# Performance work log

Measured on AMD Instinct MI355X. Metric: run time of the kernel, lower is better.

## Reference

```python
import jax, jax.numpy as jnp
import numpy as np
from jax import lax

B, S = 4, 2048
HIDDEN = 1024
OUT = 1024
NUM_TABLE = 64
CODE_LEN = 10
TABLE_SIZE = 2 ** CODE_LEN  # 1024
TOTAL_DIM = NUM_TABLE * CODE_LEN  # 640


def setup_inputs() -> dict:
    key = jax.random.key(0)
    k1, k2, k3, k4, k5 = jax.random.split(key, 5)
    hidden_states = jax.random.normal(k1, (B, S, HIDDEN), dtype=jnp.float32)
    # nn.Linear(hidden_size, total_dim): weight [total_dim, hidden] in torch; store as [hidden, total_dim]
    W_proj = jax.random.normal(k2, (HIDDEN, TOTAL_DIM), dtype=jnp.float32) * (1.0 / np.sqrt(HIDDEN))
    b_proj = jax.random.normal(k3, (TOTAL_DIM,), dtype=jnp.float32) * 0.01
    tables = 0.02 * jax.random.normal(k4, (NUM_TABLE * TABLE_SIZE, OUT), dtype=jnp.float32)
    bias = 0.001 * jax.random.normal(k5, (OUT,), dtype=jnp.float32)
    return {"hidden_states": hidden_states, "W_proj": W_proj, "b_proj": b_proj,
            "tables": tables, "bias": bias}


def reference(hidden_states, W_proj, b_proj, tables, bias):
    other_shape = hidden_states.shape[:-1]
    x = hidden_states.reshape(-1, HIDDEN)  # [N, H], N = B*S
    # Hashing: dense projection then per-table code/score
    z = x @ W_proj + b_proj                       # [N, total_dim]
    z = z.reshape(-1, NUM_TABLE, CODE_LEN)        # [N, T, L]
    t = jnp.tanh(jnp.abs(z))
    score = jnp.prod((1.0 + t) * 0.5, axis=-1)    # [N, T] prob of selected bucket
    pow2 = (2 ** jnp.arange(CODE_LEN, dtype=jnp.int32))
    code = jnp.sum((z > 0).astype(jnp.int32) * pow2, axis=-1)  # [N, T] in [0, TABLE_SIZE)

    # Gather + weighted sum over tables, streamed with scan to avoid [N, T, OUT]
    tabs = tables.reshape(NUM_TABLE, TABLE_SIZE, OUT)
    code_t = code.T    # [T, N]
    score_t = score.T  # [T, N]

    def body(acc, inp):
        tab, idx, w = inp  # tab [TABLE_SIZE, OUT], idx [N], w [N]
        return acc + tab[idx] * w[:, None], None

    acc0 = jnp.zeros((x.shape[0], OUT), dtype=hidden_states.dtype)
    out, _ = lax.scan(body, acc0, (tabs, code_t, score_t))
    out = out + bias
    return out.reshape(*other_shape, OUT)
```

## Files before the change

### kernel.cpp

```cpp
#include <hip/hip_runtime.h>
#include <cstddef>
#include <cstdint>

#define HIDDEN    1024
#define OUTD      1024
#define NUM_TABLE 64
#define CODE_LEN  10
#define TABLE_SZ  1024
#define TOTAL_DIM 640

#define TAU   1e-3f
#define FCAP  65536u

typedef float  fx4    __attribute__((ext_vector_type(4)));
typedef ushort ux4    __attribute__((ext_vector_type(4)));
typedef ushort ux8    __attribute__((ext_vector_type(8)));
typedef short  bf16x8 __attribute__((ext_vector_type(8)));
typedef float  f32x4  __attribute__((ext_vector_type(4)));

struct bfp { ushort hi, lo; };
static __device__ __forceinline__ bfp split2(float v) {
    uint32_t u  = __float_as_uint(v);
    float    fh = __uint_as_float(u & 0xFFFF0000u);
    uint32_t ul = __float_as_uint(v - fh);
    bfp r; r.hi = (ushort)(u >> 16); r.lo = (ushort)(ul >> 16);
    return r;
}
static __device__ __forceinline__ ushort f2bf(float f) {
    uint32_t u = __float_as_uint(f);
    return (ushort)((u + 0x7FFFu + ((u >> 16) & 1u)) >> 16);
}

__global__ __launch_bounds__(256)
void split_wt(const float* __restrict__ W, ushort* __restrict__ wht, ushort* __restrict__ wlt)
{
    __shared__ float t[32][33];
    const int d0 = blockIdx.x * 32, k0 = blockIdx.y * 32;
    const int lx = threadIdx.x & 31, ly = threadIdx.x >> 5;
    #pragma unroll
    for (int i = 0; i < 32; i += 8)
        t[ly + i][lx] = W[(size_t)(k0 + ly + i) * TOTAL_DIM + d0 + lx];
    __syncthreads();
    #pragma unroll
    for (int i = 0; i < 32; i += 8) {
        bfp s = split2(t[lx][ly + i]);
        size_t o = (size_t)(d0 + ly + i) * HIDDEN + k0 + lx;
        wht[o] = s.hi; wlt[o] = s.lo;
    }
}

#define GBM 128
#define GBN 128
#define GBK 32
#define LDK 40

__global__ __launch_bounds__(256)
void gemm_mfma(const float* __restrict__ x, const ushort* __restrict__ wht,
               const ushort* __restrict__ wlt, const float* __restrict__ bproj,
               float* __restrict__ z)
{
    __shared__ ushort Ah[GBM][LDK];
    __shared__ ushort Al[GBM][LDK];
    __shared__ ushort Bh[GBN][LDK];
    __shared__ ushort Bl[GBN][LDK];

    const int tid  = threadIdx.x;
    const int lane = tid & 63, wid = tid >> 6;
    const int wr = wid >> 1, wc = wid & 1;
    const int brow = blockIdx.x * GBM;
    const int bcol = blockIdx.y * GBN;
    const int fr = lane & 15, fq = lane >> 4;

    f32x4 acc[4][4] = {};

    for (int k0 = 0; k0 < HIDDEN; k0 += GBK) {
        #pragma unroll
        for (int i = 0; i < 4; ++i) {
            int c = tid + i * 256;
            int r = c >> 3, kc = (c & 7) * 4;
            fx4 v = *(const fx4*)&x[(size_t)(brow + r) * HIDDEN + k0 + kc];
            bfp s0 = split2(v.x), s1 = split2(v.y), s2 = split2(v.z), s3 = split2(v.w);
            ux4 h, l;
            h.x = s0.hi; l.x = s0.lo;
            h.y = s1.hi; l.y = s1.lo;
            h.z = s2.hi; l.z = s2.lo;
            h.w = s3.hi; l.w = s3.lo;
            *(ux4*)&Ah[r][kc] = h;
            *(ux4*)&Al[r][kc] = l;
        }
        #pragma unroll
        for (int i = 0; i < 2; ++i) {
            int c = tid + i * 256;
            int nr = c >> 2, kc = (c & 3) * 8;
            size_t o = (size_t)(bcol + nr) * HIDDEN + k0 + kc;
            *(ux8*)&Bh[nr][kc] = *(const ux8*)&wht[o];
            *(ux8*)&Bl[nr][kc] = *(const ux8*)&wlt[o];
        }
        __syncthreads();

        bf16x8 ah[4], al[4], bh[4], bl[4];
        #pragma unroll
        for (int m = 0; m < 4; ++m) {
            ah[m] = *(const bf16x8*)&Ah[wr * 64 + m * 16 + fr][fq * 8];
            al[m] = *(const bf16x8*)&Al[wr * 64 + m * 16 + fr][fq * 8];
        }
        #pragma unroll
        for (int n = 0; n < 4; ++n) {
            bh[n] = *(const bf16x8*)&Bh[wc * 64 + n * 16 + fr][fq * 8];
            bl[n] = *(const bf16x8*)&Bl[wc * 64 + n * 16 + fr][fq * 8];
        }
        #pragma unroll
        for (int m = 0; m < 4; ++m)
            #pragma unroll
            for (int n = 0; n < 4; ++n) {
                acc[m][n] = __builtin_amdgcn_mfma_f32_16x16x32_bf16(ah[m], bh[n], acc[m][n], 0, 0, 0);
                acc[m][n] = __builtin_amdgcn_mfma_f32_16x16x32_bf16(ah[m], bl[n], acc[m][n], 0, 0, 0);
                acc[m][n] = __builtin_amdgcn_mfma_f32_16x16x32_bf16(al[m], bh[n], acc[m][n], 0, 0, 0);
            }
        __syncthreads();
    }

    #pragma unroll
    for (int n = 0; n < 4; ++n) {
        int col = bcol + wc * 64 + n * 16 + fr;
        float bb = bproj[col];
        #pragma unroll
        for (int m = 0; m < 4; ++m) {
            int rbase = brow + wr * 64 + m * 16 + fq * 4;
            #pragma unroll
            for (int j = 0; j < 4; ++j)
                z[(size_t)(rbase + j) * TOTAL_DIM + col] = acc[m][n][j] + bb;
        }
    }
}

__global__ __launch_bounds__(256)
void code_score2(const float* __restrict__ z, int* __restrict__ code,
                 float* __restrict__ score, uint32_t* __restrict__ flags,
                 uint32_t* __restrict__ cnt, int NT)
{
    int idx = blockIdx.x * 256 + threadIdx.x;
    if (idx >= NT) return;
    int n = idx >> 6;
    int t = idx & 63;
    const float* zp = z + (size_t)n * TOTAL_DIM + t * CODE_LEN;
    float s = 1.0f;
    int   c = 0;
    #pragma unroll
    for (int i = 0; i < CODE_LEN; ++i) {
        float v = zp[i];
        if (fabsf(v) < TAU) {
            uint32_t slot = atomicAdd(cnt, 1u);
            if (slot < FCAP) flags[slot] = (uint32_t)(n * TOTAL_DIM + t * CODE_LEN + i);
        }
        s *= 0.5f * (1.0f + tanhf(fabsf(v)));
        c |= (v > 0.0f) ? (1 << i) : 0;
    }
    code[idx]  = c;
    score[idx] = s;
}

__global__ __launch_bounds__(256)
void fixz(const float* __restrict__ x, const float* __restrict__ W,
          const float* __restrict__ bproj, const float* __restrict__ z,
          int* __restrict__ code, const uint32_t* __restrict__ flags,
          const uint32_t* __restrict__ cnt)
{
    const int lane = threadIdx.x & 63;
    const int gw   = (blockIdx.x * 256 + threadIdx.x) >> 6;
    const int nw   = (gridDim.x * 256) >> 6;
    uint32_t count = *cnt;
    if (count > FCAP) count = FCAP;

    for (uint32_t f = gw; f < count; f += nw) {
        uint32_t e = flags[f];
        int n = e / TOTAL_DIM, d = e % TOTAL_DIM;
        const float* xr = x + (size_t)n * HIDDEN;
        float p = 0.0f;
        #pragma unroll
        for (int j = 0; j < 16; ++j) {
            int k = lane + j * 64;
            p = fmaf(xr[k], W[(size_t)k * TOTAL_DIM + d], p);
        }
        #pragma unroll
        for (int off = 32; off; off >>= 1) p += __shfl_xor(p, off);
        float v = p + bproj[d];
        if (lane == 0) {
            float vold = z[e];
            if ((v > 0.0f) != (vold > 0.0f)) {
                int t = d / CODE_LEN, i = d % CODE_LEN;
                atomicXor(&code[n * NUM_TABLE + t], 1 << i);
            }
        }
    }
}

__global__ __launch_bounds__(256)
void convert_tables(const float* __restrict__ t, ushort* __restrict__ o, int n4)
{
    const fx4* tp = (const fx4*)t;
    int stride = gridDim.x * 256;
    for (int i = blockIdx.x * 256 + threadIdx.x; i < n4; i += stride) {
        fx4 v = __builtin_nontemporal_load(&tp[i]);
        ux4 u;
        u.x = f2bf(v.x); u.y = f2bf(v.y); u.z = f2bf(v.z); u.w = f2bf(v.w);
        *(ux4*)&o[(size_t)i * 4] = u;
    }
}

__global__ __launch_bounds__(256)
void gather_sum_bf16(const ushort* __restrict__ btab, const float* __restrict__ bias,
                     const int* __restrict__ code, const float* __restrict__ score,
                     float* __restrict__ out)
{
    __shared__ int   sc[NUM_TABLE];
    __shared__ float sw[NUM_TABLE];

    const int n   = blockIdx.x;
    const int tid = threadIdx.x;

    if (tid < NUM_TABLE) {
        sc[tid] = code[n * NUM_TABLE + tid];
        sw[tid] = score[n * NUM_TABLE + tid];
    }
    __syncthreads();

    float4 acc = *(const float4*)&bias[tid * 4];

    #pragma unroll 4
    for (int t = 0; t < NUM_TABLE; ++t) {
        const ux4 v = *(const ux4*)&btab[((size_t)(t * TABLE_SZ + sc[t])) * OUTD + tid * 4];
        float w = sw[t];
        acc.x += w * __uint_as_float((uint32_t)v.x << 16);
        acc.y += w * __uint_as_float((uint32_t)v.y << 16);
        acc.z += w * __uint_as_float((uint32_t)v.z << 16);
        acc.w += w * __uint_as_float((uint32_t)v.w << 16);
    }

    *(float4*)&out[(size_t)n * OUTD + tid * 4] = acc;
}

#define BM 64
#define BN 64
#define BK 32
__global__ __launch_bounds__(256)
void gemm_proj(const float* __restrict__ x, const float* __restrict__ W,
               const float* __restrict__ bproj, float* __restrict__ z)
{
    __shared__ float As[BK][BM + 4];
    __shared__ float Bs[BK][BN];
    const int tid  = threadIdx.x;
    const int brow = blockIdx.x * BM;
    const int bcol = blockIdx.y * BN;
    const int tr   = tid >> 4;
    const int tc   = tid & 15;
    float acc[4][4] = {};
    for (int k0 = 0; k0 < HIDDEN; k0 += BK) {
        #pragma unroll
        for (int i = 0; i < 2; ++i) {
            int lin = tid + i * 256;
            int r = lin >> 3, c8 = lin & 7;
            float4 a = *(const float4*)&x[(size_t)(brow + r) * HIDDEN + k0 + c8 * 4];
            As[c8 * 4 + 0][r] = a.x; As[c8 * 4 + 1][r] = a.y;
            As[c8 * 4 + 2][r] = a.z; As[c8 * 4 + 3][r] = a.w;
        }
        #pragma unroll
        for (int i = 0; i < 2; ++i) {
            int lin = tid + i * 256;
            int kk = lin >> 4, m4 = lin & 15;
            *(float4*)&Bs[kk][m4 * 4] =
                *(const float4*)&W[(size_t)(k0 + kk) * TOTAL_DIM + bcol + m4 * 4];
        }
        __syncthreads();
        #pragma unroll
        for (int kk = 0; kk < BK; ++kk) {
            float4 a = *(const float4*)&As[kk][tr * 4];
            float4 b = *(const float4*)&Bs[kk][tc * 4];
            acc[0][0] += a.x * b.x; acc[0][1] += a.x * b.y; acc[0][2] += a.x * b.z; acc[0][3] += a.x * b.w;
            acc[1][0] += a.y * b.x; acc[1][1] += a.y * b.y; acc[1][2] += a.y * b.z; acc[1][3] += a.y * b.w;
            acc[2][0] += a.z * b.x; acc[2][1] += a.z * b.y; acc[2][2] += a.z * b.z; acc[2][3] += a.z * b.w;
            acc[3][0] += a.w * b.x; acc[3][1] += a.w * b.y; acc[3][2] += a.w * b.z; acc[3][3] += a.w * b.w;
        }
        __syncthreads();
    }
    float4 bb = *(const float4*)&bproj[bcol + tc * 4];
    #pragma unroll
    for (int i = 0; i < 4; ++i) {
        int r = brow + tr * 4 + i;
        float4 o = {acc[i][0] + bb.x, acc[i][1] + bb.y, acc[i][2] + bb.z, acc[i][3] + bb.w};
        *(float4*)&z[(size_t)r * TOTAL_DIM + bcol + tc * 4] = o;
    }
}

__global__ __launch_bounds__(256)
void code_score(const float* __restrict__ z, int* __restrict__ code,
                float* __restrict__ score, int NT)
{
    int idx = blockIdx.x * 256 + threadIdx.x;
    if (idx >= NT) return;
    int n = idx >> 6, t = idx & 63;
    const float* zp = z + (size_t)n * TOTAL_DIM + t * CODE_LEN;
    float s = 1.0f; int c = 0;
    #pragma unroll
    for (int i = 0; i < CODE_LEN; ++i) {
        float v = zp[i];
        s *= 0.5f * (1.0f + tanhf(fabsf(v)));
        c |= (v > 0.0f) ? (1 << i) : 0;
    }
    code[idx] = c; score[idx] = s;
}

__global__ __launch_bounds__(256)
void gather_sum_f32(const float* __restrict__ tables, const float* __restrict__ bias,
                    const int* __restrict__ code, const float* __restrict__ score,
                    float* __restrict__ out)
{
    __shared__ int   sc[NUM_TABLE];
    __shared__ float sw[NUM_TABLE];
    const int n = blockIdx.x, tid = threadIdx.x;
    if (tid < NUM_TABLE) {
        sc[tid] = code[n * NUM_TABLE + tid];
        sw[tid] = score[n * NUM_TABLE + tid];
    }
    __syncthreads();
    float4 acc = *(const float4*)&bias[tid * 4];
    #pragma unroll 4
    for (int t = 0; t < NUM_TABLE; ++t) {
        const float* row = tables + ((size_t)(t * TABLE_SZ + sc[t])) * OUTD;
        float4 v = *(const float4*)&row[tid * 4];
        float w = sw[t];
        acc.x += v.x * w; acc.y += v.y * w; acc.z += v.z * w; acc.w += v.w * w;
    }
    *(float4*)&out[(size_t)n * OUTD + tid * 4] = acc;
}

extern "C" void kernel_launch(void* const* d_in, const int* in_sizes, int n_in,
                              void* d_out, int out_size, void* d_ws, size_t ws_size,
                              hipStream_t stream) {
    const float* x      = (const float*)d_in[0];
    const float* W      = (const float*)d_in[1];
    const float* bproj  = (const float*)d_in[2];
    const float* tables = (const float*)d_in[3];
    const float* bias   = (const float*)d_in[4];
    float* out = (float*)d_out;

    const int N = in_sizes[0] / HIDDEN;

    char* ws = (char*)d_ws;
    size_t off_z     = 0;
    size_t off_code  = off_z + (size_t)N * TOTAL_DIM * sizeof(float);
    size_t off_score = off_code + (size_t)N * NUM_TABLE * sizeof(int);
    size_t off_btab  = off_score + (size_t)N * NUM_TABLE * sizeof(float);
    size_t tab_elems = (size_t)NUM_TABLE * TABLE_SZ * OUTD;
    size_t need      = off_btab + tab_elems * sizeof(ushort);

    float*  z     = (float*)(ws + off_z);
    int*    code  = (int*)(ws + off_code);
    float*  score = (float*)(ws + off_score);
    ushort* btab  = (ushort*)(ws + off_btab);
    uint32_t* flags = (uint32_t*)(ws + off_btab);
    uint32_t* cnt   = (uint32_t*)(ws + off_btab + (size_t)FCAP * 4);
    ushort*   wht   = (ushort*)(ws + off_btab + (1u << 20));
    ushort*   wlt   = (ushort*)(ws + off_btab + (3u << 20));

    int NT = N * NUM_TABLE;

    if (ws_size >= need) {
        dim3 gw(TOTAL_DIM / 32, HIDDEN / 32);
        split_wt<<<gw, 256, 0, stream>>>(W, wht, wlt);

        dim3 g1(N / GBM, TOTAL_DIM / GBN);
        gemm_mfma<<<g1, 256, 0, stream>>>(x, wht, wlt, bproj, z);

        (void)hipMemsetAsync(cnt, 0, 4, stream);
        code_score2<<<(NT + 255) / 256, 256, 0, stream>>>(z, code, score, flags, cnt, NT);
        fixz<<<512, 256, 0, stream>>>(x, W, bproj, z, code, flags, cnt);

        convert_tables<<<2048, 256, 0, stream>>>(tables, btab, (int)(tab_elems / 4));
        gather_sum_bf16<<<N, 256, 0, stream>>>(btab, bias, code, score, out);
    } else {
        dim3 g1(N / BM, TOTAL_DIM / BN);
        gemm_proj<<<g1, 256, 0, stream>>>(x, W, bproj, z);
        code_score<<<(NT + 255) / 256, 256, 0, stream>>>(z, code, score, NT);
        gather_sum_f32<<<N, 256, 0, stream>>>(tables, bias, code, score, out);
    }
}
```

Baseline: 344.9 us.

## Fuse table conversion into GEMM launch and split gather into column halves

The bf16 table conversion now runs as extra blocks inside the projection GEMM launch, so the memory-bound conversion can overlap the compute-bound GEMM instead of running as a separate kernel. The converted tables are stored as two column halves of 512, and the gather runs as two 128-thread launches, one per half, so each pass touches a smaller working set that may stay in cache. The risks are that conversion blocks compete with the GEMM for CUs, that the gather needs an extra launch and rereads code and score, and that the workspace layout grows.

```diff
diff --git a/kernel.cpp b/kernel.cpp
--- a/kernel.cpp
+++ b/kernel.cpp
@@ -53,22 +53,46 @@
 #define GBN 128
 #define GBK 32
 #define LDK 40
-
-__global__ __launch_bounds__(256)
-void gemm_mfma(const float* __restrict__ x, const ushort* __restrict__ wht,
-               const ushort* __restrict__ wlt, const float* __restrict__ bproj,
-               float* __restrict__ z)
+#define GEMM_MB (8192 / GBM)
+#define GEMM_NB (TOTAL_DIM / GBN)
+#define GEMM_BLKS (GEMM_MB * GEMM_NB)
+#define CONV_BLKS 1024
+
+__global__ __launch_bounds__(256)
+void gemm_convert(const float* __restrict__ x, const ushort* __restrict__ wht,
+                  const ushort* __restrict__ wlt, const float* __restrict__ bproj,
+                  float* __restrict__ z,
+                  const float* __restrict__ tables,
+                  ushort* __restrict__ btabA, ushort* __restrict__ btabB)
 {
     __shared__ ushort Ah[GBM][LDK];
     __shared__ ushort Al[GBM][LDK];
     __shared__ ushort Bh[GBN][LDK];
     __shared__ ushort Bl[GBN][LDK];
 
-    const int tid  = threadIdx.x;
+    const int gb  = blockIdx.x;
+    const int tid = threadIdx.x;
+
+    if (gb >= GEMM_BLKS) {
+        const int n4 = NUM_TABLE * TABLE_SZ * (OUTD / 4);
+        const fx4* tp = (const fx4*)tables;
+        const int stride = CONV_BLKS * 256;
+        for (int i = (gb - GEMM_BLKS) * 256 + tid; i < n4; i += stride) {
+            fx4 v = __builtin_nontemporal_load(&tp[i]);
+            ux4 u;
+            u.x = f2bf(v.x); u.y = f2bf(v.y); u.z = f2bf(v.z); u.w = f2bf(v.w);
+            int row = i >> 8;
+            int cg  = i & 255;
+            if (cg < 128) *(ux4*)&btabA[(size_t)row * 512 + cg * 4]         = u;
+            else          *(ux4*)&btabB[(size_t)row * 512 + (cg - 128) * 4] = u;
+        }
+        return;
+    }
+
     const int lane = tid & 63, wid = tid >> 6;
     const int wr = wid >> 1, wc = wid & 1;
-    const int brow = blockIdx.x * GBM;
-    const int bcol = blockIdx.y * GBN;
+    const int brow = (gb % GEMM_MB) * GBM;
+    const int bcol = (gb / GEMM_MB) * GBN;
     const int fr = lane & 15, fq = lane >> 4;
 
     f32x4 acc[4][4] = {};
@@ -195,23 +219,10 @@
     }
 }
 
-__global__ __launch_bounds__(256)
-void convert_tables(const float* __restrict__ t, ushort* __restrict__ o, int n4)
-{
-    const fx4* tp = (const fx4*)t;
-    int stride = gridDim.x * 256;
-    for (int i = blockIdx.x * 256 + threadIdx.x; i < n4; i += stride) {
-        fx4 v = __builtin_nontemporal_load(&tp[i]);
-        ux4 u;
-        u.x = f2bf(v.x); u.y = f2bf(v.y); u.z = f2bf(v.z); u.w = f2bf(v.w);
-        *(ux4*)&o[(size_t)i * 4] = u;
-    }
-}
-
-__global__ __launch_bounds__(256)
-void gather_sum_bf16(const ushort* __restrict__ btab, const float* __restrict__ bias,
-                     const int* __restrict__ code, const float* __restrict__ score,
-                     float* __restrict__ out)
+__global__ __launch_bounds__(128)
+void gather_half(const ushort* __restrict__ btabH, const float* __restrict__ bias,
+                 const int* __restrict__ code, const float* __restrict__ score,
+                 float* __restrict__ out, int colbase)
 {
     __shared__ int   sc[NUM_TABLE];
     __shared__ float sw[NUM_TABLE];
@@ -225,11 +236,11 @@
     }
     __syncthreads();
 
-    float4 acc = *(const float4*)&bias[tid * 4];
+    float4 acc = *(const float4*)&bias[colbase + tid * 4];
 
     #pragma unroll 4
     for (int t = 0; t < NUM_TABLE; ++t) {
-        const ux4 v = *(const ux4*)&btab[((size_t)(t * TABLE_SZ + sc[t])) * OUTD + tid * 4];
+        const ux4 v = *(const ux4*)&btabH[((size_t)(t * TABLE_SZ + sc[t])) * 512 + tid * 4];
         float w = sw[t];
         acc.x += w * __uint_as_float((uint32_t)v.x << 16);
         acc.y += w * __uint_as_float((uint32_t)v.y << 16);
@@ -237,7 +248,7 @@
         acc.w += w * __uint_as_float((uint32_t)v.w << 16);
     }
 
-    *(float4*)&out[(size_t)n * OUTD + tid * 4] = acc;
+    *(float4*)&out[(size_t)n * OUTD + colbase + tid * 4] = acc;
 }
 
 #define BM 64
@@ -348,36 +359,42 @@
 
     char* ws = (char*)d_ws;
     size_t off_z     = 0;
-    size_t off_code  = off_z + (size_t)N * TOTAL_DIM * sizeof(float);
-    size_t off_score = off_code + (size_t)N * NUM_TABLE * sizeof(int);
-    size_t off_btab  = off_score + (size_t)N * NUM_TABLE * sizeof(float);
-    size_t tab_elems = (size_t)NUM_TABLE * TABLE_SZ * OUTD;
-    size_t need      = off_btab + tab_elems * sizeof(ushort);
-
-    float*  z     = (float*)(ws + off_z);
-    int*    code  = (int*)(ws + off_code);
-    float*  score = (float*)(ws + off_score);
-    ushort* btab  = (ushort*)(ws + off_btab);
-    uint32_t* flags = (uint32_t*)(ws + off_btab);
-    uint32_t* cnt   = (uint32_t*)(ws + off_btab + (size_t)FCAP * 4);
-    ushort*   wht   = (ushort*)(ws + off_btab + (1u << 20));
-    ushort*   wlt   = (ushort*)(ws + off_btab + (3u << 20));
+    size_t off_code  = off_z     + (size_t)N * TOTAL_DIM * sizeof(float);
+    size_t off_score = off_code  + (size_t)N * NUM_TABLE * sizeof(int);
+    size_t off_wht   = off_score + (size_t)N * NUM_TABLE * sizeof(float);
+    size_t off_wlt   = off_wht   + (size_t)TOTAL_DIM * HIDDEN * sizeof(ushort);
+    size_t off_flags = off_wlt   + (size_t)TOTAL_DIM * HIDDEN * sizeof(ushort);
+    size_t off_cnt   = off_flags + (size_t)FCAP * sizeof(uint32_t);
+    size_t off_btabA = (off_cnt + 4 + 255) & ~(size_t)255;
+    size_t half_b    = (size_t)NUM_TABLE * TABLE_SZ * 512 * sizeof(ushort);
+    size_t off_btabB = off_btabA + half_b;
+    size_t need      = off_btabB + half_b;
+
+    float*    z     = (float*)(ws + off_z);
+    int*      code  = (int*)(ws + off_code);
+    float*    score = (float*)(ws + off_score);
+    ushort*   wht   = (ushort*)(ws + off_wht);
+    ushort*   wlt   = (ushort*)(ws + off_wlt);
+    uint32_t* flags = (uint32_t*)(ws + off_flags);
+    uint32_t* cnt   = (uint32_t*)(ws + off_cnt);
+    ushort*   btabA = (ushort*)(ws + off_btabA);
+    ushort*   btabB = (ushort*)(ws + off_btabB);
 
     int NT = N * NUM_TABLE;
 
     if (ws_size >= need) {
         dim3 gw(TOTAL_DIM / 32, HIDDEN / 32);
         split_wt<<<gw, 256, 0, stream>>>(W, wht, wlt);
-
-        dim3 g1(N / GBM, TOTAL_DIM / GBN);
-        gemm_mfma<<<g1, 256, 0, stream>>>(x, wht, wlt, bproj, z);
-
         (void)hipMemsetAsync(cnt, 0, 4, stream);
+
+        gemm_convert<<<GEMM_BLKS + CONV_BLKS, 256, 0, stream>>>(
+            x, wht, wlt, bproj, z, tables, btabA, btabB);
+
         code_score2<<<(NT + 255) / 256, 256, 0, stream>>>(z, code, score, flags, cnt, NT);
         fixz<<<512, 256, 0, stream>>>(x, W, bproj, z, code, flags, cnt);
 
-        convert_tables<<<2048, 256, 0, stream>>>(tables, btab, (int)(tab_elems / 4));
-        gather_sum_bf16<<<N, 256, 0, stream>>>(btab, bias, code, score, out);
+        gather_half<<<N, 128, 0, stream>>>(btabA, bias, code, score, out, 0);
+        gather_half<<<N, 128, 0, stream>>>(btabB, bias, code, score, out, 512);
     } else {
         dim3 g1(N / BM, TOTAL_DIM / BN);
         gemm_proj<<<g1, 256, 0, stream>>>(x, W, bproj, z);
```

New measurement: 365.2 us. +5.9%, slower.
